# Performance work log

Measured on AMD Instinct MI355X. Metric: run time of the kernel, lower is better.

Reference implementation:

```python
import jax, jax.numpy as jnp
import numpy as np
from jax import lax

B, C, M, TDIM, NUM_TASKS = 4, 128, 6, 64, 1
HL, HH = 128, 64
PROTO_LAMBDA = 5.0

def _gelu(x):
    return jax.nn.gelu(x, approximate=False)

def _lin(x, w, b):
    return x @ w.T + b

def _conv(x, w, b=None, groups=1, pad=0):
    y = lax.conv_general_dilated(x, w, (1, 1), [(pad, pad), (pad, pad)],
                                 feature_group_count=groups,
                                 dimension_numbers=('NCHW', 'OIHW', 'NCHW'))
    if b is not None:
        y = y + b[None, :, None, None]
    return y

def _gn(x, g, b, groups, eps=1e-5):
    Bb, Cc, H, W = x.shape
    xg = x.reshape(Bb, groups, -1)
    mu = xg.mean(-1, keepdims=True)
    var = ((xg - mu) ** 2).mean(-1, keepdims=True)
    xn = ((xg - mu) * lax.rsqrt(var + eps)).reshape(Bb, Cc, H, W)
    return xn * g[None, :, None, None] + b[None, :, None, None]

def _norm(x, axis=-1):
    return x / jnp.maximum(jnp.linalg.norm(x, axis=axis, keepdims=True), 1e-12)

def _resize_ac(x, oh, ow):
    # bilinear resize, align_corners=True (matches F.interpolate)
    Bb, Cc, H, W = x.shape
    def grid(n, o):
        s = jnp.linspace(0.0, float(n - 1), o)
        i0 = jnp.floor(s).astype(jnp.int32)
        i1 = jnp.minimum(i0 + 1, n - 1)
        return i0, i1, (s - i0).astype(x.dtype)
    y0, y1, wy = grid(H, oh)
    x0, x1, wx = grid(W, ow)
    t = x[:, :, y0, :] * (1 - wy)[None, None, :, None] + x[:, :, y1, :] * wy[None, None, :, None]
    return t[:, :, :, x0] * (1 - wx)[None, None, None, :] + t[:, :, :, x1] * wx[None, None, None, :]

def _forward(x_low, x_high, task_emb, pl_w, pl_g, pl_b, ph_w, ph_g, ph_b, fu_w, fu_g, fu_b,
             pi_w1, pi_b1, pi_w2, pi_b2, se_w1, se_b1, se_g, se_be, se_w2, se_b2,
             at_in_w, at_in_b, at_out_w, at_out_b, pf_w, pf_b,
             sr_w1, sr_b1, sr_w2, sr_b2, asw, eg_w1, eg_b1, eg_w2, eg_b2, ewg_w, ewg_b,
             hd_w1, hd_b1, hd_g, hd_be, hd_w2, hd_b2, eis, sim_temp, proto_amp, task_ids):
    H, W = x_low.shape[-2:]
    x_high = _resize_ac(x_high, H, W)
    xl = _gelu(_gn(_conv(x_low, pl_w), pl_g, pl_b, 1))
    xh = _gelu(_gn(_conv(x_high, ph_w), ph_g, ph_b, 1))
    x = _gelu(_gn(_conv(jnp.concatenate([xh, xl], 1), fu_w), fu_g, fu_b, 1))
    Bb = x.shape[0]

    # prototype initialization from task embedding (first sample per task id)
    pinit = _lin(_gelu(_lin(task_emb, pi_w1, pi_b1)), pi_w2, pi_b2).reshape(Bb, 1, 2, C)
    pinit = _norm(pinit, -1)
    table = jnp.stack([pinit[jnp.argmax(task_ids == t)] for t in range(NUM_TASKS)], 0)
    protos = table[task_ids]                      # (B, n_scales=1, 2, C)
    fg = _norm(protos[:, 0, 0], -1)               # (B, C)
    bg = _norm(protos[:, 0, 1], -1)

    # single-scale encoder: grouped 3x3 conv -> GN(4) -> GELU -> 1x1 conv
    sf = _conv(x, se_w1, se_b1, groups=C // 4, pad=1)
    sf = _conv(_gelu(_gn(sf, se_g, se_be, min(4, C))), se_w2, se_b2)
    sfn = _norm(sf, axis=1)
    fused_sim = (jnp.einsum('bchw,bc->bhw', sfn, fg) - jnp.einsum('bchw,bc->bhw', sfn, bg))[:, None]

    # prototype cross-attention: 2 queries attend over HW keys, 4 heads
    feat = sf.reshape(Bb, C, H * W).transpose(0, 2, 1)
    pq = jnp.stack([fg, bg], 1)                   # (B, 2, C)
    wq, wk, wv = jnp.split(at_in_w, 3, 0)
    bq, bk, bv = jnp.split(at_in_b, 3, 0)
    nh, dh = 4, C // 4
    q = (pq @ wq.T + bq).reshape(Bb, 2, nh, dh).transpose(0, 2, 1, 3)
    k = (feat @ wk.T + bk).reshape(Bb, -1, nh, dh).transpose(0, 2, 1, 3)
    v = (feat @ wv.T + bv).reshape(Bb, -1, nh, dh).transpose(0, 2, 1, 3)
    attn = jax.nn.softmax(jnp.einsum('bhqd,bhkd->bhqk', q, k) / jnp.sqrt(jnp.float32(dh)), -1)
    att = jnp.einsum('bhqk,bhkd->bhqd', attn, v).transpose(0, 2, 1, 3).reshape(Bb, 2, C)
    att = att @ at_out_w.T + at_out_b
    fg_a, bg_a = att[:, 0], att[:, 1]
    proto_feat = _lin(jnp.concatenate([fg_a, bg_a, fg_a - bg_a], -1), pf_w, pf_b)

    # scale routing (degenerate for 1 scale but kept faithful)
    tsw = jax.nn.softmax(_lin(_gelu(_lin(task_emb, sr_w1, sr_b1)), sr_w2, sr_b2), -1)
    fsw = tsw * asw[None, :]
    fsw = fsw / fsw.sum(1, keepdims=True)

    # per-sample M-expert 3x3 depthwise kernels blended toward identity
    ek = _lin(_gelu(_lin(proto_feat, eg_w1, eg_b1)), eg_w2, eg_b2).reshape(Bb, M, C, 9)
    id9 = jnp.zeros((C, 9), x.dtype).at[:, 4].set(1.0)
    ek = ek * eis + id9[None, None] * (1 - eis)
    ew = jax.nn.softmax(_lin(proto_feat, ewg_w, ewg_b), -1)  # (B, M)

    x_enh = x * (1 + 0.5 * jax.nn.sigmoid(fused_sim))
    xp = jnp.pad(x_enh, ((0, 0), (0, 0), (1, 1), (1, 1)))
    # unfold(k=3, pad=1): tap order dy-major matches torch unfold's (B, C*9, HW)
    patches = jnp.stack([xp[:, :, dy:dy + H, dx:dx + W] for dy in range(3) for dx in range(3)], 2)  # (B,C,9,H,W)
    # fold expert mixture into a single per-sample per-channel kernel (same math, reassociated)
    w_eff = jnp.einsum('bmcr,bm->bcr', ek, ew)
    y = jnp.einsum('bcr,bcrhw->bchw', w_eff, patches)

    h = _conv(y, hd_w1, hd_b1, groups=C, pad=1)
    logits = _conv(_gelu(_gn(h, hd_g, hd_be, 1)), hd_w2, hd_b2)   # (B, num_tasks, H, W)
    idx = jnp.broadcast_to(task_ids[:, None, None, None], (Bb, 1, H, W))
    logit_task = jnp.take_along_axis(logits, idx, 1)
    sim_scaled = jnp.tanh(fused_sim / (jnp.abs(fused_sim).mean() + 1e-6) / jnp.maximum(sim_temp, 1e-3))
    logit_task = logit_task + PROTO_LAMBDA * proto_amp * sim_scaled
    pred = _resize_ac(logit_task, 512, 512)
    return pred, y, fsw

def setup_inputs():
    ks = iter(jax.random.split(jax.random.key(0), 64))
    f32 = jnp.float32
    def rnd(*s):
        return jax.random.normal(next(ks), s, f32) * 0.02
    d = {}
    d['x_low'] = jax.random.normal(next(ks), (B, 64, HL, HL), f32)
    d['x_high'] = jax.random.normal(next(ks), (B, 128, HH, HH), f32)
    d['task_emb'] = jax.random.normal(next(ks), (B, TDIM), f32)
    d['pl_w'] = rnd(64, 64, 1, 1); d['pl_g'] = jnp.ones(64, f32); d['pl_b'] = jnp.zeros(64, f32)
    d['ph_w'] = rnd(C, 128, 1, 1); d['ph_g'] = jnp.ones(C, f32); d['ph_b'] = jnp.zeros(C, f32)
    d['fu_w'] = rnd(C, C + 64, 1, 1); d['fu_g'] = jnp.ones(C, f32); d['fu_b'] = jnp.zeros(C, f32)
    d['pi_w1'] = rnd(2 * C, TDIM); d['pi_b1'] = jnp.zeros(2 * C, f32)
    d['pi_w2'] = rnd(2 * C, 2 * C); d['pi_b2'] = jnp.zeros(2 * C, f32)
    d['se_w1'] = rnd(C, 4, 3, 3); d['se_b1'] = jnp.zeros(C, f32)
    d['se_g'] = jnp.ones(C, f32); d['se_be'] = jnp.zeros(C, f32)
    d['se_w2'] = rnd(C, C, 1, 1); d['se_b2'] = jnp.zeros(C, f32)
    d['at_in_w'] = rnd(3 * C, C); d['at_in_b'] = jnp.zeros(3 * C, f32)
    d['at_out_w'] = rnd(C, C); d['at_out_b'] = jnp.zeros(C, f32)
    d['pf_w'] = rnd(C, 3 * C); d['pf_b'] = jnp.zeros(C, f32)
    d['sr_w1'] = rnd(2, TDIM); d['sr_b1'] = jnp.zeros(2, f32)
    d['sr_w2'] = rnd(1, 2); d['sr_b2'] = jnp.zeros(1, f32)
    d['asw'] = jnp.ones(1, f32)
    d['eg_w1'] = rnd(2 * C, C); d['eg_b1'] = jnp.zeros(2 * C, f32)
    d['eg_w2'] = rnd(M * C * 9, 2 * C); d['eg_b2'] = jnp.zeros(M * C * 9, f32)
    d['ewg_w'] = rnd(M, C); d['ewg_b'] = jnp.zeros(M, f32)
    d['hd_w1'] = rnd(C, 1, 3, 3); d['hd_b1'] = jnp.zeros(C, f32)
    d['hd_g'] = jnp.ones(C, f32); d['hd_be'] = jnp.zeros(C, f32)
    d['hd_w2'] = rnd(NUM_TASKS, C, 1, 1); d['hd_b2'] = jnp.zeros(NUM_TASKS, f32)
    d['eis'] = jnp.asarray(0.3, f32)
    d['sim_temp'] = jnp.asarray(0.1, f32)
    d['proto_amp'] = jnp.asarray(1.0, f32)
    d['task_ids'] = jnp.zeros((B,), jnp.int32)
    return d

def reference(x_low, x_high, task_emb, pl_w, pl_g, pl_b, ph_w, ph_g, ph_b, fu_w, fu_g, fu_b,
              pi_w1, pi_b1, pi_w2, pi_b2, se_w1, se_b1, se_g, se_be, se_w2, se_b2,
              at_in_w, at_in_b, at_out_w, at_out_b, pf_w, pf_b,
              sr_w1, sr_b1, sr_w2, sr_b2, asw, eg_w1, eg_b1, eg_w2, eg_b2, ewg_w, ewg_b,
              hd_w1, hd_b1, hd_g, hd_be, hd_w2, hd_b2, eis, sim_temp, proto_amp, task_ids):
    return _forward(x_low, x_high, task_emb, pl_w, pl_g, pl_b, ph_w, ph_g, ph_b, fu_w, fu_g, fu_b,
                    pi_w1, pi_b1, pi_w2, pi_b2, se_w1, se_b1, se_g, se_be, se_w2, se_b2,
                    at_in_w, at_in_b, at_out_w, at_out_b, pf_w, pf_b,
                    sr_w1, sr_b1, sr_w2, sr_b2, asw, eg_w1, eg_b1, eg_w2, eg_b2, ewg_w, ewg_b,
                    hd_w1, hd_b1, hd_g, hd_be, hd_w2, hd_b2, eis, sim_temp, proto_amp, task_ids)
```

## Files before the change

### kernel.cpp

```cpp
#include <hip/hip_runtime.h>
#include <math.h>

constexpr int B_ = 4;
constexpr int C_ = 128;
constexpr int HW_ = 16384;
constexpr int W_ = 128;
constexpr int M_ = 6;
constexpr int TDIM_ = 64;
constexpr int NT_ = 1;

static __device__ __forceinline__ float gelu_f(float x){
  return 0.5f * x * (1.0f + erff(x * 0.7071067811865476f));
}
static __device__ __forceinline__ int imin(int a, int b){ return a < b ? a : b; }

static __device__ __forceinline__ float block_reduce_sum256(float v, float* lds){
  int t = threadIdx.x;
  lds[t] = v; __syncthreads();
  for (int s = 128; s > 0; s >>= 1){ if (t < s) lds[t] += lds[t + s]; __syncthreads(); }
  float r = lds[0]; __syncthreads();
  return r;
}

__global__ void k_resize(const float* __restrict__ in, float* __restrict__ out,
                         int BC, int Hi, int Wi, int Ho, int Wo){
  int idx = blockIdx.x * 256 + threadIdx.x;
  int total = BC * Ho * Wo;
  if (idx >= total) return;
  int xo = idx % Wo; int yo = (idx / Wo) % Ho; int bc = idx / (Wo * Ho);
  float sy = (Ho > 1) ? yo * (float)(Hi - 1) / (float)(Ho - 1) : 0.f;
  float sx = (Wo > 1) ? xo * (float)(Wi - 1) / (float)(Wo - 1) : 0.f;
  int y0 = (int)floorf(sy); int y1 = imin(y0 + 1, Hi - 1); float wy = sy - (float)y0;
  int x0 = (int)floorf(sx); int x1 = imin(x0 + 1, Wi - 1); float wx = sx - (float)x0;
  const float* p = in + (size_t)bc * Hi * Wi;
  float a = p[y0 * Wi + x0], b = p[y1 * Wi + x0];
  float c = p[y0 * Wi + x1], d = p[y1 * Wi + x1];
  float t0 = a * (1.f - wy) + b * wy;
  float t1 = c * (1.f - wy) + d * wy;
  out[idx] = t0 * (1.f - wx) + t1 * wx;
}

__global__ void k_stat2(const float* __restrict__ ps, const float* __restrict__ pq,
                        float* __restrict__ gm, float* __restrict__ gi,
                        int nper, float nelem){
  int idx = blockIdx.x; int t = threadIdx.x;
  __shared__ float l1[128], l2[128];
  float s = 0.f, ss = 0.f;
  for (int i = t; i < nper; i += 128){ s += ps[idx * nper + i]; ss += pq[idx * nper + i]; }
  l1[t] = s; l2[t] = ss; __syncthreads();
  for (int st = 64; st > 0; st >>= 1){
    if (t < st){ l1[t] += l1[t + st]; l2[t] += l2[t + st]; }
    __syncthreads();
  }
  if (t == 0){
    float mu = l1[0] / nelem;
    float var = l2[0] / nelem - mu * mu;
    gm[idx] = mu; gi[idx] = rsqrtf(var + 1e-5f);
  }
}

__global__ void k_stat2_dual(const float* __restrict__ psA, const float* __restrict__ pqA,
                             float* __restrict__ gmA, float* __restrict__ giA, float nelemA,
                             const float* __restrict__ psB, const float* __restrict__ pqB,
                             float* __restrict__ gmB, float* __restrict__ giB, float nelemB){
  int idx = blockIdx.x; int t = threadIdx.x;
  __shared__ float l1[128], l2[128];
  const float* ps; const float* pq; float* gm; float* gi; float nelem; int id2;
  if (idx < 4){ ps = psA; pq = pqA; gm = gmA; gi = giA; nelem = nelemA; id2 = idx; }
  else        { ps = psB; pq = pqB; gm = gmB; gi = giB; nelem = nelemB; id2 = idx - 4; }
  float s = 0.f, ss = 0.f;
  for (int i = t; i < 256; i += 128){ s += ps[id2 * 256 + i]; ss += pq[id2 * 256 + i]; }
  l1[t] = s; l2[t] = ss; __syncthreads();
  for (int st = 64; st > 0; st >>= 1){
    if (t < st){ l1[t] += l1[t + st]; l2[t] += l2[t + st]; }
    __syncthreads();
  }
  if (t == 0){
    float mu = l1[0] / nelem;
    float var = l2[0] / nelem - mu * mu;
    gm[id2] = mu; gi[id2] = rsqrtf(var + 1e-5f);
  }
}

__global__ void k_wtall(const float* __restrict__ ph_w, const float* __restrict__ pl_w,
                        const float* __restrict__ fu_w, const float* __restrict__ se_w2,
                        float* __restrict__ wTph, float* __restrict__ wTpl,
                        float* __restrict__ wTfu, float* __restrict__ wTse){
  int idx = blockIdx.x * 256 + threadIdx.x;
  if (idx < 16384){
    int ci = idx / 128, co = idx % 128;
    wTph[idx] = ph_w[co * 128 + ci];
  } else if (idx < 20480){
    int r = idx - 16384; int ci = r / 64, co = r % 64;
    wTpl[r] = pl_w[co * 64 + ci];
  } else if (idx < 45056){
    int r = idx - 20480; int ci = r / 128, co = r % 128;
    wTfu[r] = fu_w[(size_t)co * 192 + ci];
  } else if (idx < 61440){
    int r = idx - 45056; int ci = r / 128, co = r % 128;
    wTse[r] = se_w2[co * 128 + ci];
  }
}

template<int CO, int CIT>
static __device__ __forceinline__ void gemm_body(
    const float* __restrict__ in1, const float* __restrict__ wT,
    float* __restrict__ out, float* __restrict__ psum, float* __restrict__ psq,
    int b, int j0, int slot, float* As, float* Bs, float* red){
  const int tid = threadIdx.x;
  const int tj = tid & 15, tco = tid >> 4;
  constexpr int CPT = CO / 16;
  constexpr int AST = CO + 4;
  float acc[CPT][4];
  #pragma unroll
  for (int i = 0; i < CPT; ++i)
    #pragma unroll
    for (int j = 0; j < 4; ++j) acc[i][j] = 0.f;

  for (int k0 = 0; k0 < CIT; k0 += 16){
    const int kk = tid >> 4;
    if constexpr (CO == 128){
      int co = (tid & 15) * 8;
      const float* wp = &wT[(size_t)(k0 + kk) * CO + co];
      *(float4*)&As[kk * AST + co] = *(const float4*)wp;
      *(float4*)&As[kk * AST + co + 4] = *(const float4*)(wp + 4);
    } else {
      int co = (tid & 15) * 4;
      *(float4*)&As[kk * AST + co] = *(const float4*)&wT[(size_t)(k0 + kk) * CO + co];
    }
    {
      int jj = (tid & 15) * 4;
      int ci = k0 + kk;
      float4 v = *(const float4*)&in1[((size_t)b * CIT + ci) * HW_ + j0 + jj];
      *(float4*)&Bs[kk * 68 + jj] = v;
    }
    __syncthreads();
    #pragma unroll
    for (int kkk = 0; kkk < 16; ++kkk){
      float4 bq = *(const float4*)&Bs[kkk * 68 + tj * 4];
      float av[CPT];
      if constexpr (CPT == 8){
        float4 a0 = *(const float4*)&As[kkk * AST + tco * 8];
        float4 a1 = *(const float4*)&As[kkk * AST + tco * 8 + 4];
        av[0] = a0.x; av[1] = a0.y; av[2] = a0.z; av[3] = a0.w;
        av[4] = a1.x; av[5] = a1.y; av[6] = a1.z; av[7] = a1.w;
      } else {
        float4 a0 = *(const float4*)&As[kkk * AST + tco * 4];
        av[0] = a0.x; av[1] = a0.y; av[2] = a0.z; av[3] = a0.w;
      }
      #pragma unroll
      for (int i = 0; i < CPT; ++i){
        acc[i][0] = fmaf(av[i], bq.x, acc[i][0]);
        acc[i][1] = fmaf(av[i], bq.y, acc[i][1]);
        acc[i][2] = fmaf(av[i], bq.z, acc[i][2]);
        acc[i][3] = fmaf(av[i], bq.w, acc[i][3]);
      }
    }
    __syncthreads();
  }
  float s = 0.f, ss = 0.f;
  #pragma unroll
  for (int i = 0; i < CPT; ++i){
    int co = tco * CPT + i;
    float4 o;
    o.x = acc[i][0]; o.y = acc[i][1]; o.z = acc[i][2]; o.w = acc[i][3];
    *(float4*)&out[((size_t)b * CO + co) * HW_ + j0 + tj * 4] = o;
    s += o.x + o.y + o.z + o.w;
    ss += o.x * o.x + o.y * o.y + o.z * o.z + o.w * o.w;
  }
  s = block_reduce_sum256(s, red);
  ss = block_reduce_sum256(ss, red);
  if (tid == 0){ psum[slot] = s; psq[slot] = ss; }
}

__global__ __launch_bounds__(256, 4) void k_gemm_dual(
    const float* __restrict__ in_ph, const float* __restrict__ wT_ph,
    float* __restrict__ out_ph, float* __restrict__ psA, float* __restrict__ pqA,
    const float* __restrict__ in_pl, const float* __restrict__ wT_pl,
    float* __restrict__ out_pl, float* __restrict__ psB, float* __restrict__ pqB){
  __shared__ float As[16 * 132];
  __shared__ float Bs[16 * 68];
  __shared__ float red[256];
  int b = blockIdx.x;
  if (blockIdx.y < 256){
    int yb = blockIdx.y;
    gemm_body<128, 128>(in_ph, wT_ph, out_ph, psA, pqA, b, yb * 64, b * 256 + yb, As, Bs, red);
  } else {
    int yb = blockIdx.y - 256;
    gemm_body<64, 64>(in_pl, wT_pl, out_pl, psB, pqB, b, yb * 64, b * 256 + yb, As, Bs, red);
  }
}

template<int CO, int CIT>
__global__ __launch_bounds__(256, 4) void k_gemm1x1(
    const float* __restrict__ in1, const float* __restrict__ in2, int CI1,
    const float* __restrict__ wT, const float* __restrict__ bias,
    const float* __restrict__ gm1, const float* __restrict__ gi1,
    const float* __restrict__ ga1, const float* __restrict__ be1, int sh1, int ng1,
    const float* __restrict__ gm2, const float* __restrict__ gi2,
    const float* __restrict__ ga2, const float* __restrict__ be2, int sh2, int ng2,
    float* __restrict__ out, float* __restrict__ psum, float* __restrict__ psq){
  __shared__ float As[16][CO + 4];
  __shared__ float Bs[16][68];
  __shared__ float red[256];
  const int b = blockIdx.x;
  const int j0 = blockIdx.y * 64;
  const int tid = threadIdx.x;
  const int tj = tid & 15, tco = tid >> 4;
  constexpr int CPT = CO / 16;

  float acc[CPT][4];
  #pragma unroll
  for (int i = 0; i < CPT; ++i)
    #pragma unroll
    for (int j = 0; j < 4; ++j) acc[i][j] = 0.f;

  for (int k0 = 0; k0 < CIT; k0 += 16){
    const int kk = tid >> 4;
    if constexpr (CO == 128){
      int co = (tid & 15) * 8;
      const float* wp = &wT[(size_t)(k0 + kk) * CO + co];
      *(float4*)&As[kk][co] = *(const float4*)wp;
      *(float4*)&As[kk][co + 4] = *(const float4*)(wp + 4);
    } else {
      int co = (tid & 15) * 4;
      *(float4*)&As[kk][co] = *(const float4*)&wT[(size_t)(k0 + kk) * CO + co];
    }
    {
      int jj = (tid & 15) * 4;
      int ci = k0 + kk;
      float4 v;
      if (ci < CI1){
        v = *(const float4*)&in1[((size_t)b * CI1 + ci) * HW_ + j0 + jj];
        if (gm1){
          int g = ci >> sh1;
          float rs = gi1[b * ng1 + g];
          float ga = ga1[ci] * rs;
          float be = be1[ci] - gm1[b * ng1 + g] * ga;
          v.x = gelu_f(fmaf(v.x, ga, be)); v.y = gelu_f(fmaf(v.y, ga, be));
          v.z = gelu_f(fmaf(v.z, ga, be)); v.w = gelu_f(fmaf(v.w, ga, be));
        }
      } else {
        int c2 = ci - CI1;
        v = *(const float4*)&in2[((size_t)b * (CIT - CI1) + c2) * HW_ + j0 + jj];
        if (gm2){
          int g = c2 >> sh2;
          float rs = gi2[b * ng2 + g];
          float ga = ga2[c2] * rs;
          float be = be2[c2] - gm2[b * ng2 + g] * ga;
          v.x = gelu_f(fmaf(v.x, ga, be)); v.y = gelu_f(fmaf(v.y, ga, be));
          v.z = gelu_f(fmaf(v.z, ga, be)); v.w = gelu_f(fmaf(v.w, ga, be));
        }
      }
      *(float4*)&Bs[kk][jj] = v;
    }
    __syncthreads();
    #pragma unroll
    for (int kkk = 0; kkk < 16; ++kkk){
      float4 bq = *(const float4*)&Bs[kkk][tj * 4];
      float av[CPT];
      if constexpr (CPT == 8){
        float4 a0 = *(const float4*)&As[kkk][tco * 8];
        float4 a1 = *(const float4*)&As[kkk][tco * 8 + 4];
        av[0] = a0.x; av[1] = a0.y; av[2] = a0.z; av[3] = a0.w;
        av[4] = a1.x; av[5] = a1.y; av[6] = a1.z; av[7] = a1.w;
      } else {
        float4 a0 = *(const float4*)&As[kkk][tco * 4];
        av[0] = a0.x; av[1] = a0.y; av[2] = a0.z; av[3] = a0.w;
      }
      #pragma unroll
      for (int i = 0; i < CPT; ++i){
        acc[i][0] = fmaf(av[i], bq.x, acc[i][0]);
        acc[i][1] = fmaf(av[i], bq.y, acc[i][1]);
        acc[i][2] = fmaf(av[i], bq.z, acc[i][2]);
        acc[i][3] = fmaf(av[i], bq.w, acc[i][3]);
      }
    }
    __syncthreads();
  }
  float s = 0.f, ss = 0.f;
  #pragma unroll
  for (int i = 0; i < CPT; ++i){
    int co = tco * CPT + i;
    float bb = bias ? bias[co] : 0.f;
    float4 o;
    o.x = acc[i][0] + bb; o.y = acc[i][1] + bb;
    o.z = acc[i][2] + bb; o.w = acc[i][3] + bb;
    *(float4*)&out[((size_t)b * CO + co) * HW_ + j0 + tj * 4] = o;
    s += o.x + o.y + o.z + o.w;
    ss += o.x * o.x + o.y * o.y + o.z * o.z + o.w * o.w;
  }
  if (psum){
    s = block_reduce_sum256(s, red);
    ss = block_reduce_sum256(ss, red);
    if (tid == 0){
      psum[b * gridDim.y + blockIdx.y] = s;
      psq [b * gridDim.y + blockIdx.y] = ss;
    }
  }
}

__global__ __launch_bounds__(256) void k_se3(const float* __restrict__ x,
    const float* __restrict__ gm, const float* __restrict__ gi,
    const float* __restrict__ gamma, const float* __restrict__ beta,
    const float* __restrict__ w, const float* __restrict__ bias,
    float* __restrict__ out, float* __restrict__ psum, float* __restrict__ psq){
  __shared__ float xs[4][10][128];
  __shared__ float ws[144];
  __shared__ float wb[4];
  __shared__ float red[256];
  const int bgc = blockIdx.x; const int b = bgc >> 5, gc = bgc & 31;
  const int r0 = blockIdx.y * 8;
  const int tid = threadIdx.x;
  const float mu = gm[b], rs = gi[b];
  for (int ch = 0; ch < 4; ++ch){
    int c = gc * 4 + ch;
    float ga = gamma[c] * rs, be = beta[c] - mu * rs * gamma[c];
    const float* px = x + ((size_t)b * C_ + c) * HW_;
    for (int i = tid; i < 10 * 128; i += 256){
      int rr = i >> 7, cc = i & 127;
      int row = r0 - 1 + rr;
      float v = 0.f;
      if ((unsigned)row < 128u) v = gelu_f(fmaf(px[row * W_ + cc], ga, be));
      xs[ch][rr][cc] = v;
    }
  }
  if (tid < 144) ws[tid] = w[(size_t)(gc * 4) * 36 + tid];
  if (tid < 4)   wb[tid] = bias[gc * 4 + tid];
  __syncthreads();
  const int hf = tid >> 7;
  const int cc = tid & 127;
  float s = 0.f, ss = 0.f;
  for (int co_l = 0; co_l < 4; ++co_l){
    float bb = wb[co_l];
    float a0 = bb, a1 = bb, a2 = bb, a3 = bb;
    #pragma unroll
    for (int cil = 0; cil < 4; ++cil){
      float w9[9];
      #pragma unroll
      for (int i = 0; i < 9; ++i) w9[i] = ws[(co_l * 4 + cil) * 9 + i];
      #pragma unroll
      for (int q = 0; q < 6; ++q){
        int xr = 4 * hf + q;
        float mdl = xs[cil][xr][cc];
        float lft = (cc > 0)   ? xs[cil][xr][cc - 1] : 0.f;
        float rgt = (cc < 127) ? xs[cil][xr][cc + 1] : 0.f;
        if (q <= 2){
          int ky = q;       a0 = fmaf(w9[ky*3], lft, a0); a0 = fmaf(w9[ky*3+1], mdl, a0); a0 = fmaf(w9[ky*3+2], rgt, a0);
        }
        if (q >= 1 && q <= 3){
          int ky = q - 1;   a1 = fmaf(w9[ky*3], lft, a1); a1 = fmaf(w9[ky*3+1], mdl, a1); a1 = fmaf(w9[ky*3+2], rgt, a1);
        }
        if (q >= 2 && q <= 4){
          int ky = q - 2;   a2 = fmaf(w9[ky*3], lft, a2); a2 = fmaf(w9[ky*3+1], mdl, a2); a2 = fmaf(w9[ky*3+2], rgt, a2);
        }
        if (q >= 3){
          int ky = q - 3;   a3 = fmaf(w9[ky*3], lft, a3); a3 = fmaf(w9[ky*3+1], mdl, a3); a3 = fmaf(w9[ky*3+2], rgt, a3);
        }
      }
    }
    float* po = &out[((size_t)b * C_ + gc * 4 + co_l) * HW_ + (r0 + 4 * hf) * W_ + cc];
    po[0]       = a0;
    po[W_]      = a1;
    po[2 * W_]  = a2;
    po[3 * W_]  = a3;
    s += a0 + a1 + a2 + a3;
    ss += a0 * a0 + a1 * a1 + a2 * a2 + a3 * a3;
  }
  s = block_reduce_sum256(s, red);
  ss = block_reduce_sum256(ss, red);
  if (tid == 0){
    int idx = (b * 4 + (gc >> 3)) * 128 + (gc & 7) * 16 + blockIdx.y;
    psum[idx] = s; psq[idx] = ss;
  }
}

__global__ __launch_bounds__(256) void k_ydw(const float* __restrict__ x,
    const float* __restrict__ factor,
    const float* __restrict__ gm, const float* __restrict__ gi,
    const float* __restrict__ gamma, const float* __restrict__ beta,
    const float* __restrict__ w_eff, const float* __restrict__ dw_w,
    const float* __restrict__ dw_b, float* __restrict__ y_out,
    float* __restrict__ h_out, float* __restrict__ psum, float* __restrict__ psq){
  __shared__ float xs[36][128];
  __shared__ float ys[34][128];
  __shared__ float red[256];
  const int bc = blockIdx.x; const int b = bc >> 7, c = bc & 127;
  const int r0 = blockIdx.y * 32;
  const int tid = threadIdx.x;
  const float mu = gm[b], rs = gi[b];
  const float ga = gamma[c] * rs, be = beta[c] - mu * rs * gamma[c];
  const float* px = x + ((size_t)b * C_ + c) * HW_;
  const float* pf = factor + (size_t)b * HW_;
  for (int i = tid; i < 36 * 128; i += 256){
    int rr = i >> 7, cc = i & 127;
    int row = r0 - 2 + rr;
    float v = 0.f;
    if ((unsigned)row < 128u)
      v = gelu_f(fmaf(px[row * W_ + cc], ga, be)) * pf[row * W_ + cc];
    xs[rr][cc] = v;
  }
  __syncthreads();
  float w9[9];
  #pragma unroll
  for (int r = 0; r < 9; ++r) w9[r] = w_eff[b * 1152 + c * 9 + r];
  for (int i = tid; i < 34 * 128; i += 256){
    int rr = i >> 7, cc = i & 127;
    int row = r0 - 1 + rr;
    float acc = 0.f;
    if ((unsigned)row < 128u){
      #pragma unroll
      for (int ky = 0; ky < 3; ++ky){
        #pragma unroll
        for (int kx = 0; kx < 3; ++kx){
          int xc = cc + kx - 1;
          if ((unsigned)xc < 128u) acc += w9[ky * 3 + kx] * xs[rr + ky][xc];
        }
      }
    }
    ys[rr][cc] = acc;
    if (rr >= 1 && rr <= 32)
      y_out[((size_t)b * C_ + c) * HW_ + row * W_ + cc] = acc;
  }
  __syncthreads();
  float wd[9];
  #pragma unroll
  for (int r = 0; r < 9; ++r) wd[r] = dw_w[c * 9 + r];
  const float bb = dw_b[c];
  float s = 0.f, ss = 0.f;
  for (int i = tid; i < 32 * 128; i += 256){
    int rr = i >> 7, cc = i & 127;
    int row = r0 + rr;
    float acc = bb;
    #pragma unroll
    for (int ky = 0; ky < 3; ++ky){
      #pragma unroll
      for (int kx = 0; kx < 3; ++kx){
        int yc = cc + kx - 1;
        if ((unsigned)yc < 128u) acc += wd[ky * 3 + kx] * ys[rr + ky][yc];
      }
    }
    h_out[((size_t)b * C_ + c) * HW_ + row * W_ + cc] = acc;
    s += acc; ss += acc * acc;
  }
  s = block_reduce_sum256(s, red);
  ss = block_reduce_sum256(ss, red);
  if (tid == 0){
    int idx = b * 512 + c * 4 + blockIdx.y;
    psum[idx] = s; psq[idx] = ss;
  }
}

__global__ void k_pinit(const float* __restrict__ temb, const float* __restrict__ w1,
                        const float* __restrict__ b1, const float* __restrict__ w2,
                        const float* __restrict__ b2, float* __restrict__ pinit){
  int b = blockIdx.x; int t = threadIdx.x;
  __shared__ float h1[256], p2[256], nrm[2];
  float acc = b1[t];
  for (int i = 0; i < TDIM_; ++i) acc += temb[b * TDIM_ + i] * w1[t * TDIM_ + i];
  h1[t] = gelu_f(acc); __syncthreads();
  acc = b2[t];
  for (int i = 0; i < 256; ++i) acc += h1[i] * w2[t * 256 + i];
  p2[t] = acc; __syncthreads();
  if (t < 2){
    float s = 0.f;
    for (int c = 0; c < 128; ++c){ float v = p2[t * 128 + c]; s += v * v; }
    nrm[t] = fmaxf(sqrtf(s), 1e-12f);
  }
  __syncthreads();
  pinit[b * 256 + t] = p2[t] / nrm[t / 128];
}

__global__ void k_protos(const float* __restrict__ pinit, const int* __restrict__ task_ids,
                         float* __restrict__ fg, float* __restrict__ bg){
  __shared__ int tbl[NT_];
  __shared__ int src[B_];
  __shared__ float nr[B_ * 2];
  int t = threadIdx.x;
  if (t < NT_){
    int idx = 0;
    for (int b = B_ - 1; b >= 0; --b) if (task_ids[b] == t) idx = b;
    tbl[t] = idx;
  }
  __syncthreads();
  if (t < B_){
    int ti = task_ids[t]; ti = ti < 0 ? 0 : (ti >= NT_ ? NT_ - 1 : ti);
    src[t] = tbl[ti];
  }
  __syncthreads();
  if (t < 2 * B_){
    int b = t / 2, r = t % 2;
    float s = 0.f;
    for (int c = 0; c < 128; ++c){ float v = pinit[src[b] * 256 + r * 128 + c]; s += v * v; }
    nr[t] = fmaxf(sqrtf(s), 1e-12f);
  }
  __syncthreads();
  for (int i = t; i < B_ * 128; i += 256){
    int b = i / 128, c = i % 128;
    fg[i] = pinit[src[b] * 256 + c] / nr[b * 2 + 0];
    bg[i] = pinit[src[b] * 256 + 128 + c] / nr[b * 2 + 1];
  }
}

__global__ void k_qk(const float* __restrict__ fg, const float* __restrict__ bg,
                     const float* __restrict__ at_in_w, const float* __restrict__ at_in_b,
                     float* __restrict__ qkvec, float* __restrict__ kdot){
  int b = blockIdx.x, t = threadIdx.x;
  __shared__ float pq[256], qf[256];
  pq[t] = (t < 128) ? fg[b * 128 + t] : bg[b * 128 + (t - 128)];
  __syncthreads();
  {
    int qi = t / 128, o = t % 128;
    float acc = at_in_b[o];
    const float* wr = at_in_w + (size_t)o * 128;
    for (int c = 0; c < 128; ++c) acc += wr[c] * pq[qi * 128 + c];
    qf[qi * 128 + o] = acc;
  }
  __syncthreads();
  for (int e = t; e < 1024; e += 256){
    int p = e / 128, c = e % 128, qi = p / 4, h = p % 4;
    float acc = 0.f;
    for (int d = 0; d < 32; ++d)
      acc += qf[qi * 128 + h * 32 + d] * at_in_w[(size_t)(128 + h * 32 + d) * 128 + c];
    qkvec[b * 1024 + e] = acc;
  }
  if (t < 8){
    int qi = t / 4, h = t % 4;
    float acc = 0.f;
    for (int d = 0; d < 32; ++d) acc += qf[qi * 128 + h * 32 + d] * at_in_b[128 + h * 32 + d];
    kdot[b * 8 + t] = acc;
  }
}

__global__ __launch_bounds__(256) void k_simscores(const float* __restrict__ sf,
                          const float* __restrict__ fg, const float* __restrict__ bg,
                          const float* __restrict__ qkvec, const float* __restrict__ kdot,
                          float* __restrict__ sim, float* __restrict__ factor,
                          float* __restrict__ scores, float* __restrict__ psim){
  int b = blockIdx.x; int j0 = blockIdx.y * 64;
  int t = threadIdx.x;
  int g = t >> 6, jl = t & 63;
  int j = j0 + jl;
  __shared__ float L[10 * 128];
  __shared__ float part[11 * 256];
  __shared__ float red64[64];
  for (int i = t; i < 1280; i += 256){
    int r = i >> 7, c = i & 127;
    L[i] = (r == 0) ? fg[b * 128 + c]
         : (r == 1) ? bg[b * 128 + c]
                    : qkvec[b * 1024 + (r - 2) * 128 + c];
  }
  __syncthreads();
  const float* p = sf + (size_t)b * C_ * HW_ + j;
  float a0=0,a1=0,q0=0,q1=0,q2=0,q3=0,q4=0,q5=0,q6=0,q7=0,nn=0;
  int c0 = g * 32;
  #pragma unroll 8
  for (int c = c0; c < c0 + 32; ++c){
    float v = p[(size_t)c * HW_];
    nn += v * v;
    a0 += L[c] * v;          a1 += L[128 + c] * v;
    q0 += L[256 + c] * v;    q1 += L[384 + c] * v;
    q2 += L[512 + c] * v;    q3 += L[640 + c] * v;
    q4 += L[768 + c] * v;    q5 += L[896 + c] * v;
    q6 += L[1024 + c] * v;   q7 += L[1152 + c] * v;
  }
  part[0 * 256 + t] = nn;  part[1 * 256 + t] = a0;  part[2 * 256 + t] = a1;
  part[3 * 256 + t] = q0;  part[4 * 256 + t] = q1;  part[5 * 256 + t] = q2;
  part[6 * 256 + t] = q3;  part[7 * 256 + t] = q4;  part[8 * 256 + t] = q5;
  part[9 * 256 + t] = q6;  part[10 * 256 + t] = q7;
  __syncthreads();
  float sv = 0.f;
  if (t < 64){
    float tot[11];
    #pragma unroll
    for (int i = 0; i < 11; ++i)
      tot[i] = part[i * 256 + t] + part[i * 256 + t + 64]
             + part[i * 256 + t + 128] + part[i * 256 + t + 192];
    float inv = 1.f / fmaxf(sqrtf(tot[0]), 1e-12f);
    sv = (tot[1] - tot[2]) * inv;
    sim[b * HW_ + j0 + t] = sv;
    factor[b * HW_ + j0 + t] = 1.f + 0.5f / (1.f + expf(-sv));
    const float scale = 0.17677669529663689f;
    #pragma unroll
    for (int pp = 0; pp < 8; ++pp)
      scores[((size_t)(b * 8 + pp)) * HW_ + j0 + t] = (tot[3 + pp] + kdot[b * 8 + pp]) * scale;
  }
  __syncthreads();
  if (t < 64) red64[t] = fabsf(sv);
  __syncthreads();
  for (int s2 = 32; s2 > 0; s2 >>= 1){
    if (t < s2) red64[t] += red64[t + s2];
    __syncthreads();
  }
  if (t == 0) psim[b * 256 + blockIdx.y] = red64[0];
}

__global__ void k_smstats(const float* __restrict__ scores, float* __restrict__ smax,
                          float* __restrict__ ssum){
  __shared__ float lds[256];
  int row = blockIdx.x;
  const float* p = scores + (size_t)row * HW_;
  float m = -1e30f;
  for (int j = threadIdx.x; j < HW_; j += 256) m = fmaxf(m, p[j]);
  lds[threadIdx.x] = m; __syncthreads();
  for (int s = 128; s > 0; s >>= 1){
    if (threadIdx.x < s) lds[threadIdx.x] = fmaxf(lds[threadIdx.x], lds[threadIdx.x + s]);
    __syncthreads();
  }
  m = lds[0]; __syncthreads();
  float z = 0.f;
  for (int j = threadIdx.x; j < HW_; j += 256) z += expf(p[j] - m);
  z = block_reduce_sum256(z, lds);
  if (threadIdx.x == 0){ smax[row] = m; ssum[row] = z; }
}

__global__ void k_wsum(const float* __restrict__ sf, const float* __restrict__ scores,
                       const float* __restrict__ smax, const float* __restrict__ ssum,
                       float* __restrict__ wsum4){
  int bc = blockIdx.x; int b = bc / C_, c = bc % C_;
  int chunk = blockIdx.y;
  __shared__ float lds[8 * 256];
  __shared__ float mr[8], zr[8];
  if (threadIdx.x < 8){
    mr[threadIdx.x] = smax[b * 8 + threadIdx.x];
    zr[threadIdx.x] = 1.f / ssum[b * 8 + threadIdx.x];
  }
  __syncthreads();
  const float* p = sf + (size_t)bc * HW_;
  const float* sc = scores + (size_t)b * 8 * HW_;
  int j0 = chunk * (HW_ / 4), j1 = j0 + HW_ / 4;
  float acc[8] = {0,0,0,0,0,0,0,0};
  for (int j = j0 + threadIdx.x; j < j1; j += 256){
    float v = p[j];
    #pragma unroll
    for (int pp = 0; pp < 8; ++pp)
      acc[pp] = fmaf(expf(sc[(size_t)pp * HW_ + j] - mr[pp]) * zr[pp], v, acc[pp]);
  }
  #pragma unroll
  for (int pp = 0; pp < 8; ++pp) lds[pp * 256 + threadIdx.x] = acc[pp];
  __syncthreads();
  for (int s = 128; s > 0; s >>= 1){
    if (threadIdx.x < s){
      #pragma unroll
      for (int pp = 0; pp < 8; ++pp) lds[pp * 256 + threadIdx.x] += lds[pp * 256 + threadIdx.x + s];
    }
    __syncthreads();
  }
  if (threadIdx.x < 8)
    wsum4[chunk * 4096 + b * 1024 + threadIdx.x * 128 + c] = lds[threadIdx.x * 256];
}

__global__ void k_small(const float* __restrict__ wsum4, const float* __restrict__ at_in_w,
                        const float* __restrict__ at_in_b, const float* __restrict__ at_out_w,
                        const float* __restrict__ at_out_b, const float* __restrict__ pf_w,
                        const float* __restrict__ pf_b, const float* __restrict__ eg_w1,
                        const float* __restrict__ eg_b1, const float* __restrict__ ewg_w,
                        const float* __restrict__ ewg_b, float* __restrict__ eg1_out,
                        float* __restrict__ ew_out){
  int b = blockIdx.x; int t = threadIdx.x;
  __shared__ float wsl[1024], att[256], ao[256], pf[128], ewl[8];
  for (int i = t; i < 1024; i += 256)
    wsl[i] = wsum4[b * 1024 + i] + wsum4[4096 + b * 1024 + i]
           + wsum4[8192 + b * 1024 + i] + wsum4[12288 + b * 1024 + i];
  __syncthreads();
  {
    int qi = t / 128, o = t % 128, h = o / 32, d = o % 32, p = qi * 4 + h;
    float acc = at_in_b[256 + h * 32 + d];
    const float* wr = at_in_w + (size_t)(256 + h * 32 + d) * 128;
    for (int c = 0; c < 128; ++c) acc += wr[c] * wsl[p * 128 + c];
    att[qi * 128 + o] = acc;
  }
  __syncthreads();
  {
    int qi = t / 128, o = t % 128;
    float acc = at_out_b[o];
    const float* wr = at_out_w + (size_t)o * 128;
    for (int c = 0; c < 128; ++c) acc += wr[c] * att[qi * 128 + c];
    ao[qi * 128 + o] = acc;
  }
  __syncthreads();
  if (t < 128){
    float acc = pf_b[t];
    const float* wr = pf_w + (size_t)t * 384;
    for (int c = 0; c < 128; ++c){
      float fa = ao[c], ba = ao[128 + c];
      acc += wr[c] * fa + wr[128 + c] * ba + wr[256 + c] * (fa - ba);
    }
    pf[t] = acc;
  }
  __syncthreads();
  {
    float acc = eg_b1[t];
    const float* wr = eg_w1 + (size_t)t * 128;
    for (int c = 0; c < 128; ++c) acc += wr[c] * pf[c];
    eg1_out[b * 256 + t] = gelu_f(acc);
  }
  if (t < M_){
    float acc = ewg_b[t];
    const float* wr = ewg_w + (size_t)t * 128;
    for (int c = 0; c < 128; ++c) acc += wr[c] * pf[c];
    ewl[t] = acc;
  }
  __syncthreads();
  if (t == 0){
    float m = -1e30f;
    for (int i = 0; i < M_; ++i) m = fmaxf(m, ewl[i]);
    float z = 0.f;
    for (int i = 0; i < M_; ++i){ ewl[i] = expf(ewl[i] - m); z += ewl[i]; }
    for (int i = 0; i < M_; ++i) ew_out[b * M_ + i] = ewl[i] / z;
  }
}

__global__ void k_weff(const float* __restrict__ eg1, const float* __restrict__ ew,
                       const float* __restrict__ eg_w2, const float* __restrict__ eg_b2,
                       const float* __restrict__ eis_p, float* __restrict__ w_eff){
  int b = blockIdx.x; int cr = blockIdx.y * 256 + threadIdx.x;
  __shared__ float e1[256]; __shared__ float ewl[M_];
  e1[threadIdx.x] = eg1[b * 256 + threadIdx.x];
  if (threadIdx.x < M_) ewl[threadIdx.x] = ew[b * M_ + threadIdx.x];
  __syncthreads();
  if (cr >= C_ * 9) return;
  int c = cr / 9, r = cr % 9;
  float eis = eis_p[0];
  float acc = 0.f;
  for (int m = 0; m < M_; ++m){
    size_t row = ((size_t)m * C_ + c) * 9 + r;
    float v = eg_b2[row];
    const float* wr = eg_w2 + row * 256;
    for (int i = 0; i < 256; ++i) v += wr[i] * e1[i];
    float ekv = v * eis + ((r == 4) ? (1.f - eis) : 0.f);
    acc += ewl[m] * ekv;
  }
  w_eff[b * (C_ * 9) + cr] = acc;
}

__global__ __launch_bounds__(256) void k_logits(const float* __restrict__ h,
                         const float* __restrict__ gmean,
                         const float* __restrict__ ginv, const float* __restrict__ hd_g,
                         const float* __restrict__ hd_be, const float* __restrict__ hd_w2,
                         const float* __restrict__ hd_b2, const int* __restrict__ task_ids,
                         float* __restrict__ logits){
  int b = blockIdx.x; int j0 = blockIdx.y * 64;
  int t = threadIdx.x;
  int g = t >> 6, jl = t & 63;
  int it = task_ids[b]; it = it < 0 ? 0 : (it >= NT_ ? NT_ - 1 : it);
  __shared__ float wg[128], wb[128], w2[128];
  __shared__ float part[256];
  if (t < 128){
    wg[t] = hd_g[t];
    wb[t] = hd_be[t];
    w2[t] = hd_w2[it * C_ + t];
  }
  __syncthreads();
  float mu = gmean[b], rs = ginv[b];
  const float* p = h + (size_t)b * C_ * HW_ + j0 + jl;
  float acc = 0.f;
  int c0 = g * 32;
  #pragma unroll 8
  for (int c = c0; c < c0 + 32; ++c){
    float v = p[(size_t)c * HW_];
    v = (v - mu) * rs * wg[c] + wb[c];
    acc += w2[c] * gelu_f(v);
  }
  part[t] = acc;
  __syncthreads();
  if (t < 64){
    float tot = part[t] + part[t + 64] + part[t + 128] + part[t + 192] + hd_b2[it];
    logits[b * HW_ + j0 + t] = tot;
  }
}

__global__ void k_final(float* __restrict__ logits, const float* __restrict__ sim,
                        const float* __restrict__ psim, const float* __restrict__ sim_temp,
                        const float* __restrict__ proto_amp,
                        const float* __restrict__ asw, float* __restrict__ fsw_out){
  __shared__ float red[256];
  float s = psim[threadIdx.x] + psim[256 + threadIdx.x]
          + psim[512 + threadIdx.x] + psim[768 + threadIdx.x];
  s = block_reduce_sum256(s, red);
  int idx = blockIdx.x * 256 + threadIdx.x;
  float mean = s / (float)(B_ * HW_);
  float denom = mean + 1e-6f;
  float temp = fmaxf(sim_temp[0], 0.001f);
  float v = tanhf(sim[idx] / denom / temp);
  logits[idx] += 5.0f * proto_amp[0] * v;
  if (blockIdx.x == 0 && threadIdx.x < B_){
    float a = 1.0f * asw[0];
    fsw_out[threadIdx.x] = a / a;
  }
}

extern "C" void kernel_launch(void* const* d_in, const int* in_sizes, int n_in,
                              void* d_out, int out_size, void* d_ws, size_t ws_size,
                              hipStream_t stream){
  const float* x_low   = (const float*)d_in[0];
  const float* x_high  = (const float*)d_in[1];
  const float* temb    = (const float*)d_in[2];
  const float* pl_w    = (const float*)d_in[3];
  const float* pl_g    = (const float*)d_in[4];
  const float* pl_b    = (const float*)d_in[5];
  const float* ph_w    = (const float*)d_in[6];
  const float* ph_g    = (const float*)d_in[7];
  const float* ph_b    = (const float*)d_in[8];
  const float* fu_w    = (const float*)d_in[9];
  const float* fu_g    = (const float*)d_in[10];
  const float* fu_b    = (const float*)d_in[11];
  const float* pi_w1   = (const float*)d_in[12];
  const float* pi_b1   = (const float*)d_in[13];
  const float* pi_w2   = (const float*)d_in[14];
  const float* pi_b2   = (const float*)d_in[15];
  const float* se_w1   = (const float*)d_in[16];
  const float* se_b1   = (const float*)d_in[17];
  const float* se_g    = (const float*)d_in[18];
  const float* se_be   = (const float*)d_in[19];
  const float* se_w2   = (const float*)d_in[20];
  const float* se_b2   = (const float*)d_in[21];
  const float* at_in_w = (const float*)d_in[22];
  const float* at_in_b = (const float*)d_in[23];
  const float* at_out_w= (const float*)d_in[24];
  const float* at_out_b= (const float*)d_in[25];
  const float* pf_w    = (const float*)d_in[26];
  const float* pf_b    = (const float*)d_in[27];
  const float* asw     = (const float*)d_in[32];
  const float* eg_w1   = (const float*)d_in[33];
  const float* eg_b1   = (const float*)d_in[34];
  const float* eg_w2   = (const float*)d_in[35];
  const float* eg_b2   = (const float*)d_in[36];
  const float* ewg_w   = (const float*)d_in[37];
  const float* ewg_b   = (const float*)d_in[38];
  const float* hd_w1   = (const float*)d_in[39];
  const float* hd_b1   = (const float*)d_in[40];
  const float* hd_g    = (const float*)d_in[41];
  const float* hd_be   = (const float*)d_in[42];
  const float* hd_w2   = (const float*)d_in[43];
  const float* hd_b2   = (const float*)d_in[44];
  const float* eis     = (const float*)d_in[45];
  const float* sim_temp= (const float*)d_in[46];
  const float* proto_amp=(const float*)d_in[47];
  const int*   task_ids= (const int*)d_in[48];

  float* ws = (float*)d_ws;
  const size_t BIG = (size_t)B_ * C_ * HW_;
  float* S0 = ws;
  float* S1 = ws + BIG;
  float* S2 = ws + 2 * BIG;
  float* scores = ws + 3 * BIG;
  float* sm = scores + (size_t)B_ * 8 * HW_;
  float* sim     = sm;             sm += (size_t)B_ * HW_;
  float* factor  = sm;             sm += (size_t)B_ * HW_;
  float* logitsb = sm;             sm += (size_t)B_ * HW_;
  float* psA = sm; sm += 1024; float* pqA = sm; sm += 1024;
  float* psB = sm; sm += 1024; float* pqB = sm; sm += 1024;
  float* psC = sm; sm += 1024; float* pqC = sm; sm += 1024;
  float* ps3 = sm; sm += 2048; float* pq3 = sm; sm += 2048;
  float* psH = sm; sm += 2048; float* pqH = sm; sm += 2048;
  float* gmA = sm; sm += 4;  float* giA = sm; sm += 4;
  float* gmB = sm; sm += 4;  float* giB = sm; sm += 4;
  float* gmC = sm; sm += 4;  float* giC = sm; sm += 4;
  float* gm3 = sm; sm += 16; float* gi3 = sm; sm += 16;
  float* gmH = sm; sm += 4;  float* giH = sm; sm += 4;
  float* pinitb  = sm;             sm += 1024;
  float* fgb     = sm;             sm += 512;
  float* bgb     = sm;             sm += 512;
  float* qkvecb  = sm;             sm += 4096;
  float* kdotb   = sm;             sm += 32;
  float* smaxb   = sm;             sm += 32;
  float* ssumb   = sm;             sm += 32;
  float* wsum4b  = sm;             sm += 16384;
  float* eg1b    = sm;             sm += 1024;
  float* ewb     = sm;             sm += 32;
  float* weffb   = sm;             sm += 4608;
  float* psimb   = sm;             sm += 1024;
  float* wTph    = sm;             sm += 128 * 128;
  float* wTpl    = sm;             sm += 64 * 64;
  float* wTfu    = sm;             sm += 192 * 128;
  float* wTse    = sm;             sm += 128 * 128;

  float* pred_out = (float*)d_out;
  float* y_out    = pred_out + (size_t)B_ * 512 * 512;
  float* fsw_out  = y_out + BIG;

  dim3 blk(256);
  const float* NF = nullptr;
  float* NFm = nullptr;

  k_wtall<<<240, blk, 0, stream>>>(ph_w, pl_w, fu_w, se_w2, wTph, wTpl, wTfu, wTse);
  k_resize<<<(unsigned)(BIG / 256), blk, 0, stream>>>(x_high, S0, B_ * C_, 64, 64, 128, 128);
  k_gemm_dual<<<dim3(B_, 512), blk, 0, stream>>>(S0, wTph, S1, psA, pqA,
                                                 x_low, wTpl, S2, psB, pqB);
  k_stat2_dual<<<8, 128, 0, stream>>>(psA, pqA, gmA, giA, (float)(128 * HW_),
                                      psB, pqB, gmB, giB, (float)(64 * HW_));
  k_gemm1x1<128,192><<<dim3(B_, 256), blk, 0, stream>>>(S1, S2, 128, wTfu, NF,
      gmA,giA,ph_g,ph_b,7,1, gmB,giB,pl_g,pl_b,6,1, S0, psC, pqC);
  k_stat2<<<B_, 128, 0, stream>>>(psC, pqC, gmC, giC, 256, (float)(128 * HW_));
  k_se3<<<dim3(B_ * 32, 16), blk, 0, stream>>>(S0, gmC, giC, fu_g, fu_b,
      se_w1, se_b1, S2, ps3, pq3);
  k_stat2<<<B_ * 4, 128, 0, stream>>>(ps3, pq3, gm3, gi3, 128, (float)(32 * HW_));
  k_gemm1x1<128,128><<<dim3(B_, 256), blk, 0, stream>>>(S2, NF, 128, wTse, se_b2,
      gm3,gi3,se_g,se_be,5,4, NF,NF,NF,NF,0,0, S1, NFm, NFm);
  k_pinit<<<B_, blk, 0, stream>>>(temb, pi_w1, pi_b1, pi_w2, pi_b2, pinitb);
  k_protos<<<1, blk, 0, stream>>>(pinitb, task_ids, fgb, bgb);
  k_qk<<<B_, blk, 0, stream>>>(fgb, bgb, at_in_w, at_in_b, qkvecb, kdotb);
  k_simscores<<<dim3(B_, 256), blk, 0, stream>>>(S1, fgb, bgb, qkvecb, kdotb,
                                                 sim, factor, scores, psimb);
  k_smstats<<<B_ * 8, blk, 0, stream>>>(scores, smaxb, ssumb);
  k_wsum<<<dim3(B_ * C_, 4), blk, 0, stream>>>(S1, scores, smaxb, ssumb, wsum4b);
  k_small<<<B_, blk, 0, stream>>>(wsum4b, at_in_w, at_in_b, at_out_w, at_out_b,
                                  pf_w, pf_b, eg_w1, eg_b1, ewg_w, ewg_b, eg1b, ewb);
  k_weff<<<dim3(B_, 5), blk, 0, stream>>>(eg1b, ewb, eg_w2, eg_b2, eis, weffb);
  k_ydw<<<dim3(B_ * C_, 4), blk, 0, stream>>>(S0, factor, gmC, giC, fu_g, fu_b,
      weffb, hd_w1, hd_b1, y_out, S2, psH, pqH);
  k_stat2<<<B_, 128, 0, stream>>>(psH, pqH, gmH, giH, 512, (float)(128 * HW_));
  k_logits<<<dim3(B_, 256), blk, 0, stream>>>(S2, gmH, giH, hd_g, hd_be, hd_w2, hd_b2,
                                              task_ids, logitsb);
  k_final<<<(unsigned)((size_t)B_ * HW_ / 256), blk, 0, stream>>>(logitsb, sim, psimb,
                                                                  sim_temp, proto_amp,
                                                                  asw, fsw_out);
  k_resize<<<(unsigned)((size_t)B_ * 512 * 512 / 256), blk, 0, stream>>>(logitsb, pred_out,
                                                                          B_, 128, 128, 512, 512);
}
```

Measured before the change: 462.2 us.

## Run high-branch 1x1 conv before upsampling and split softmax stats into chunks

Because a 1x1 conv and bilinear resize are both linear, the high-resolution branch now applies the conv at 64x64 and resizes the result to 128x128. GroupNorm statistics are gathered in a new fused resize kernel. This cuts the GEMM work for that branch by a factor of four and removes one full-size intermediate pass. The softmax max/sum reduction is also split into 8 chunks per row so more blocks run, and k_wsum merges the partial results with log-sum-exp rescaling. The conv-before-resize reordering changes floating-point rounding slightly.

```diff
diff --git a/kernel.cpp b/kernel.cpp
--- a/kernel.cpp
+++ b/kernel.cpp
@@ -38,6 +38,35 @@
   float t0 = a * (1.f - wy) + b * wy;
   float t1 = c * (1.f - wy) + d * wy;
   out[idx] = t0 * (1.f - wx) + t1 * wx;
+}
+
+__global__ void k_resize_stat(const float* __restrict__ in,
+                              float* __restrict__ out,
+                              float* __restrict__ psum, float* __restrict__ psq){
+  int b = blockIdx.x; int y = blockIdx.y;
+  int t = threadIdx.x;
+  __shared__ float red[256];
+  float s = 0.f, ss = 0.f;
+  const float SC = 63.f / 127.f;
+  for (int k = 0; k < 32; ++k){
+    int e = y * 8192 + k * 256 + t;
+    int c = e >> 14, p = e & 16383;
+    int yo = p >> 7, xo = p & 127;
+    float sy = yo * SC, sx = xo * SC;
+    int y0 = (int)sy; int y1 = imin(y0 + 1, 63); float wy = sy - (float)y0;
+    int x0 = (int)sx; int x1 = imin(x0 + 1, 63); float wx = sx - (float)x0;
+    const float* pp = in + ((size_t)b * 128 + c) * 4096;
+    float a = pp[y0 * 64 + x0], bb = pp[y1 * 64 + x0];
+    float cc = pp[y0 * 64 + x1], d = pp[y1 * 64 + x1];
+    float t0 = a * (1.f - wy) + bb * wy;
+    float t1 = cc * (1.f - wy) + d * wy;
+    float v = t0 * (1.f - wx) + t1 * wx;
+    out[((size_t)b * 128 + c) * (size_t)HW_ + p] = v;
+    s += v; ss += v * v;
+  }
+  s = block_reduce_sum256(s, red);
+  ss = block_reduce_sum256(ss, red);
+  if (t == 0){ psum[b * 256 + y] = s; psq[b * 256 + y] = ss; }
 }
 
 __global__ void k_stat2(const float* __restrict__ ps, const float* __restrict__ pq,
@@ -102,7 +131,7 @@
   }
 }
 
-template<int CO, int CIT>
+template<int CO, int CIT, int HWN>
 static __device__ __forceinline__ void gemm_body(
     const float* __restrict__ in1, const float* __restrict__ wT,
     float* __restrict__ out, float* __restrict__ psum, float* __restrict__ psq,
@@ -131,7 +160,7 @@
     {
       int jj = (tid & 15) * 4;
       int ci = k0 + kk;
-      float4 v = *(const float4*)&in1[((size_t)b * CIT + ci) * HW_ + j0 + jj];
+      float4 v = *(const float4*)&in1[((size_t)b * CIT + ci) * HWN + j0 + jj];
       *(float4*)&Bs[kk * 68 + jj] = v;
     }
     __syncthreads();
@@ -164,7 +193,7 @@
     int co = tco * CPT + i;
     float4 o;
     o.x = acc[i][0]; o.y = acc[i][1]; o.z = acc[i][2]; o.w = acc[i][3];
-    *(float4*)&out[((size_t)b * CO + co) * HW_ + j0 + tj * 4] = o;
+    *(float4*)&out[((size_t)b * CO + co) * HWN + j0 + tj * 4] = o;
     s += o.x + o.y + o.z + o.w;
     ss += o.x * o.x + o.y * o.y + o.z * o.z + o.w * o.w;
   }
@@ -175,19 +204,19 @@
 
 __global__ __launch_bounds__(256, 4) void k_gemm_dual(
     const float* __restrict__ in_ph, const float* __restrict__ wT_ph,
-    float* __restrict__ out_ph, float* __restrict__ psA, float* __restrict__ pqA,
+    float* __restrict__ out_ph, float* __restrict__ psD, float* __restrict__ pqD,
     const float* __restrict__ in_pl, const float* __restrict__ wT_pl,
     float* __restrict__ out_pl, float* __restrict__ psB, float* __restrict__ pqB){
   __shared__ float As[16 * 132];
   __shared__ float Bs[16 * 68];
   __shared__ float red[256];
   int b = blockIdx.x;
-  if (blockIdx.y < 256){
+  if (blockIdx.y < 64){
     int yb = blockIdx.y;
-    gemm_body<128, 128>(in_ph, wT_ph, out_ph, psA, pqA, b, yb * 64, b * 256 + yb, As, Bs, red);
+    gemm_body<128, 128, 4096>(in_ph, wT_ph, out_ph, psD, pqD, b, yb * 64, b * 64 + yb, As, Bs, red);
   } else {
-    int yb = blockIdx.y - 256;
-    gemm_body<64, 64>(in_pl, wT_pl, out_pl, psB, pqB, b, yb * 64, b * 256 + yb, As, Bs, red);
+    int yb = blockIdx.y - 64;
+    gemm_body<64, 64, 16384>(in_pl, wT_pl, out_pl, psB, pqB, b, yb * 64, b * 256 + yb, As, Bs, red);
   }
 }
 
@@ -595,13 +624,13 @@
   if (t == 0) psim[b * 256 + blockIdx.y] = red64[0];
 }
 
-__global__ void k_smstats(const float* __restrict__ scores, float* __restrict__ smax,
-                          float* __restrict__ ssum){
+__global__ void k_smpart(const float* __restrict__ scores, float* __restrict__ pm,
+                         float* __restrict__ pz){
   __shared__ float lds[256];
-  int row = blockIdx.x;
-  const float* p = scores + (size_t)row * HW_;
+  int row = blockIdx.x; int chunk = blockIdx.y;
+  const float* p = scores + (size_t)row * HW_ + chunk * 2048;
   float m = -1e30f;
-  for (int j = threadIdx.x; j < HW_; j += 256) m = fmaxf(m, p[j]);
+  for (int j = threadIdx.x; j < 2048; j += 256) m = fmaxf(m, p[j]);
   lds[threadIdx.x] = m; __syncthreads();
   for (int s = 128; s > 0; s >>= 1){
     if (threadIdx.x < s) lds[threadIdx.x] = fmaxf(lds[threadIdx.x], lds[threadIdx.x + s]);
@@ -609,21 +638,28 @@
   }
   m = lds[0]; __syncthreads();
   float z = 0.f;
-  for (int j = threadIdx.x; j < HW_; j += 256) z += expf(p[j] - m);
+  for (int j = threadIdx.x; j < 2048; j += 256) z += expf(p[j] - m);
   z = block_reduce_sum256(z, lds);
-  if (threadIdx.x == 0){ smax[row] = m; ssum[row] = z; }
+  if (threadIdx.x == 0){ pm[row * 8 + chunk] = m; pz[row * 8 + chunk] = z; }
 }
 
 __global__ void k_wsum(const float* __restrict__ sf, const float* __restrict__ scores,
-                       const float* __restrict__ smax, const float* __restrict__ ssum,
+                       const float* __restrict__ pm, const float* __restrict__ pz,
                        float* __restrict__ wsum4){
   int bc = blockIdx.x; int b = bc / C_, c = bc % C_;
   int chunk = blockIdx.y;
   __shared__ float lds[8 * 256];
   __shared__ float mr[8], zr[8];
   if (threadIdx.x < 8){
-    mr[threadIdx.x] = smax[b * 8 + threadIdx.x];
-    zr[threadIdx.x] = 1.f / ssum[b * 8 + threadIdx.x];
+    int r = b * 8 + threadIdx.x;
+    float m = -1e30f;
+    #pragma unroll
+    for (int i = 0; i < 8; ++i) m = fmaxf(m, pm[r * 8 + i]);
+    float z = 0.f;
+    #pragma unroll
+    for (int i = 0; i < 8; ++i) z += pz[r * 8 + i] * expf(pm[r * 8 + i] - m);
+    mr[threadIdx.x] = m;
+    zr[threadIdx.x] = 1.f / z;
   }
   __syncthreads();
   const float* p = sf + (size_t)bc * HW_;
@@ -852,6 +888,7 @@
   float* psA = sm; sm += 1024; float* pqA = sm; sm += 1024;
   float* psB = sm; sm += 1024; float* pqB = sm; sm += 1024;
   float* psC = sm; sm += 1024; float* pqC = sm; sm += 1024;
+  float* psD = sm; sm += 256;  float* pqD = sm; sm += 256;
   float* ps3 = sm; sm += 2048; float* pq3 = sm; sm += 2048;
   float* psH = sm; sm += 2048; float* pqH = sm; sm += 2048;
   float* gmA = sm; sm += 4;  float* giA = sm; sm += 4;
@@ -864,8 +901,8 @@
   float* bgb     = sm;             sm += 512;
   float* qkvecb  = sm;             sm += 4096;
   float* kdotb   = sm;             sm += 32;
-  float* smaxb   = sm;             sm += 32;
-  float* ssumb   = sm;             sm += 32;
+  float* pmb     = sm;             sm += 256;
+  float* pzb     = sm;             sm += 256;
   float* wsum4b  = sm;             sm += 16384;
   float* eg1b    = sm;             sm += 1024;
   float* ewb     = sm;             sm += 32;
@@ -885,9 +922,9 @@
   float* NFm = nullptr;
 
   k_wtall<<<240, blk, 0, stream>>>(ph_w, pl_w, fu_w, se_w2, wTph, wTpl, wTfu, wTse);
-  k_resize<<<(unsigned)(BIG / 256), blk, 0, stream>>>(x_high, S0, B_ * C_, 64, 64, 128, 128);
-  k_gemm_dual<<<dim3(B_, 512), blk, 0, stream>>>(S0, wTph, S1, psA, pqA,
+  k_gemm_dual<<<dim3(B_, 320), blk, 0, stream>>>(x_high, wTph, S0, psD, pqD,
                                                  x_low, wTpl, S2, psB, pqB);
+  k_resize_stat<<<dim3(B_, 256), blk, 0, stream>>>(S0, S1, psA, pqA);
   k_stat2_dual<<<8, 128, 0, stream>>>(psA, pqA, gmA, giA, (float)(128 * HW_),
                                       psB, pqB, gmB, giB, (float)(64 * HW_));
   k_gemm1x1<128,192><<<dim3(B_, 256), blk, 0, stream>>>(S1, S2, 128, wTfu, NF,
@@ -903,8 +940,8 @@
   k_qk<<<B_, blk, 0, stream>>>(fgb, bgb, at_in_w, at_in_b, qkvecb, kdotb);
   k_simscores<<<dim3(B_, 256), blk, 0, stream>>>(S1, fgb, bgb, qkvecb, kdotb,
                                                  sim, factor, scores, psimb);
-  k_smstats<<<B_ * 8, blk, 0, stream>>>(scores, smaxb, ssumb);
-  k_wsum<<<dim3(B_ * C_, 4), blk, 0, stream>>>(S1, scores, smaxb, ssumb, wsum4b);
+  k_smpart<<<dim3(B_ * 8, 8), blk, 0, stream>>>(scores, pmb, pzb);
+  k_wsum<<<dim3(B_ * C_, 4), blk, 0, stream>>>(S1, scores, pmb, pzb, wsum4b);
   k_small<<<B_, blk, 0, stream>>>(wsum4b, at_in_w, at_in_b, at_out_w, at_out_b,
                                   pf_w, pf_b, eg_w1, eg_b1, ewg_w, ewg_b, eg1b, ewb);
   k_weff<<<dim3(B_, 5), blk, 0, stream>>>(eg1b, ewb, eg_w2, eg_b2, eis, weffb);
```

Measured after the change: 420.1 us. -9.1%, faster.
